# Kernel optimization log

Measured on AMD Instinct MI355X. Metric: run time of the kernel, lower is better.

## Reference

```python
import jax, jax.numpy as jnp
import numpy as np

B, T, D_MODEL, D_HEAD = 4, 4096, 512, 64  # batch, token_depth, token_len, d_head
D_K = 64
NEG = -1.0e9  # mask fill value used by the torch module


def setup_inputs() -> dict:
    key = jax.random.key(0)
    kx, kq, kk, kv = jax.random.split(key, 4)
    x = jax.random.normal(kx, (B, T, D_MODEL), dtype=jnp.float32)
    # nn.Linear(token_len, d_head, bias=False) -> weight shape [d_head, token_len]
    Wq = jax.random.normal(kq, (D_HEAD, D_MODEL), dtype=jnp.float32) * 0.02
    Wk = jax.random.normal(kk, (D_HEAD, D_MODEL), dtype=jnp.float32) * 0.02
    Wv = jax.random.normal(kv, (D_HEAD, D_MODEL), dtype=jnp.float32) * 0.02
    return {"x": x, "Wq": Wq, "Wk": Wk, "Wv": Wv}


def reference(x, Wq, Wk, Wv):
    # q/k/v projections: y = x @ W.T  (Linear with bias=False)
    q = jnp.einsum("btd,hd->bth", x, Wq)  # [B,T,D_HEAD]
    k = jnp.einsum("btd,hd->bth", x, Wk)
    v = jnp.einsum("btd,hd->bth", x, Wv)

    scores = jnp.einsum("bth,bsh->bts", q, k)  # [B,T,T]

    # additive causal mask: upper triangle (diagonal=1) filled with -1e9
    t_idx = jnp.arange(T)
    mask = jnp.where(t_idx[None, :] > t_idx[:, None], NEG, 0.0).astype(scores.dtype)
    scores = scores + mask[None, :, :]

    sqrt_dk = jnp.sqrt(jnp.asarray(D_K, dtype=scores.dtype))
    # NOTE: original code applies softmax over dim=1 (the query axis), not -1.
    attn = jax.nn.softmax(scores / sqrt_dk, axis=1)
    out = jnp.einsum("bts,bsh->bth", attn, v)  # [B,T,D_HEAD]
    return out
```

## Files before the change

### kernel.cpp

```cpp
#include <hip/hip_runtime.h>

#define B_ 4
#define T_ 4096
#define DM 512
#define DH 64
#define CS 512
#define CTS 1024

typedef short short8 __attribute__((ext_vector_type(8)));
typedef short bf16x4 __attribute__((ext_vector_type(4)));
typedef float f32x4 __attribute__((ext_vector_type(4)));
typedef float float8 __attribute__((ext_vector_type(8)));

__device__ inline short f2bf(float f) {
    unsigned u = __float_as_uint(f);
    u += 0x7fffu + ((u >> 16) & 1u);
    return (short)(u >> 16);
}
__device__ inline float bf2f(short s) {
    return __uint_as_float(((unsigned)(unsigned short)s) << 16);
}
__device__ inline short8 cvt8(const float* p) {
    float8 v = *(const float8*)p;
    short8 r;
#pragma unroll
    for (int j = 0; j < 8; j++) r[j] = f2bf(v[j]);
    return r;
}
__device__ inline unsigned cvt_pk_bf16(float a, float b) {
    unsigned r;
    asm("v_cvt_pk_bf16_f32 %0, %1, %2" : "=v"(r) : "v"(a), "v"(b));
    return r;
}
__device__ inline bf16x4 pmask4(f32x4 d, int sbase, int t) {
    float p[4];
#pragma unroll
    for (int r = 0; r < 4; r++) {
        float e = __expf(d[r] * 0.125f);
        p[r] = (sbase + r <= t) ? e : 0.f;
    }
    union { unsigned u[2]; bf16x4 v; } z;
    z.u[0] = cvt_pk_bf16(p[0], p[1]);
    z.u[1] = cvt_pk_bf16(p[2], p[3]);
    return z.v;
}

__global__ __launch_bounds__(256) void k_wcvt(
    const float* __restrict__ Wq, const float* __restrict__ Wk,
    const float* __restrict__ Wv, short* __restrict__ wb)
{
    int e = (blockIdx.x * 256 + threadIdx.x) * 8;
    int m = e / (DH * DM);
    int off = e - m * (DH * DM);
    const float* W = (m == 0) ? Wq : (m == 1) ? Wk : Wv;
    *(short8*)(wb + e) = cvt8(W + off);
}

__global__ __launch_bounds__(256, 4) void k_proj(
    const float* __restrict__ x, const short* __restrict__ wb,
    short* __restrict__ qb, short* __restrict__ kb, short* __restrict__ vb)
{
    __shared__ short Xs[64 * 72];
    __shared__ short Ws[192 * 72];
    int tid = threadIdx.x;
    int lane = tid & 63, w = tid >> 6;
    int l16 = lane & 15, quad = lane >> 4;
    int b = blockIdx.x >> 6;
    int tile = blockIdx.x & 63;
    int t0 = tile * 64;
    long xbase = ((long)(b * T_ + t0)) * DM;

    f32x4 acc[12];
#pragma unroll
    for (int i = 0; i < 12; i++) acc[i] = (f32x4)(0.f);

    for (int kc = 0; kc < DM; kc += 64) {
#pragma unroll
        for (int p = 0; p < 2; p++) {
            int idx = p * 256 + tid;
            int row = idx >> 3, col = (idx & 7) * 8;
            *(short8*)(Xs + row * 72 + col) = cvt8(x + xbase + (long)row * DM + kc + col);
        }
#pragma unroll
        for (int p = 0; p < 6; p++) {
            int idx = p * 256 + tid;
            int row = idx >> 3, col = (idx & 7) * 8;
            *(short8*)(Ws + row * 72 + col) =
                *(const short8*)(wb + (long)row * DM + kc + col);
        }
        __syncthreads();
#pragma unroll
        for (int ks = 0; ks < 2; ks++) {
            short8 af = *(const short8*)(Xs + (w * 16 + l16) * 72 + ks * 32 + quad * 8);
#pragma unroll
            for (int hh = 0; hh < 12; hh++) {
                short8 bf = *(const short8*)(Ws + (hh * 16 + l16) * 72 + ks * 32 + quad * 8);
                acc[hh] = __builtin_amdgcn_mfma_f32_16x16x32_bf16(af, bf, acc[hh], 0, 0, 0);
            }
        }
        __syncthreads();
    }
#pragma unroll
    for (int m = 0; m < 3; m++) {
        short* outp = (m == 0) ? qb : (m == 1) ? kb : vb;
#pragma unroll
        for (int h4 = 0; h4 < 4; h4++)
#pragma unroll
            for (int r4 = 0; r4 < 4; r4++) {
                int t = t0 + w * 16 + quad * 4 + r4;
                outp[((long)(b * T_ + t)) * DH + h4 * 16 + l16] = f2bf(acc[m * 4 + h4][r4]);
            }
    }
}

__global__ __launch_bounds__(256, 4) void k_stats(
    const short* __restrict__ qb, const short* __restrict__ kb, float* __restrict__ lsum)
{
    __shared__ short Qb[128 * 72];
    int tid = threadIdx.x;
    int lane = tid & 63, w = tid >> 6;
    int l16 = lane & 15, quad = lane >> 4;
    const int NC = T_ / CTS;
    int chunk = blockIdx.x % NC;
    int st = (blockIdx.x / NC) & 31;
    int b = blockIdx.x / (NC * 32);
    int c0 = chunk * CTS, cend = c0 + CTS;
    int s0blk = st * 128;
    if (cend <= s0blk) return;
    int s0w = s0blk + w * 32;
    long bq = (long)b * T_ * DH;

    const short8* kp0 = (const short8*)(kb + bq + (long)(s0w + l16) * DH + quad * 8);
    short8 a00 = kp0[0], a01 = kp0[4];
    const short8* kp1 = (const short8*)(kb + bq + (long)(s0w + 16 + l16) * DH + quad * 8);
    short8 a10 = kp1[0], a11 = kp1[4];

    int t_lo = (c0 > s0blk) ? c0 : s0blk;
    int nsteps = (cend - t_lo) >> 7;
    float acc0[4] = {0.f, 0.f, 0.f, 0.f};
    float acc1[4] = {0.f, 0.f, 0.f, 0.f};

    for (int stp = 0; stp < nsteps; stp++) {
        int t0 = t_lo + stp * 128;
#pragma unroll
        for (int p = 0; p < 4; p++) {
            int idx = p * 256 + tid;
            int row = idx >> 3, col = idx & 7;
            *(short8*)(Qb + row * 72 + col * 8) =
                *(const short8*)(qb + bq + (long)(t0 + row) * DH + col * 8);
        }
        __syncthreads();
        for (int sub = 0; sub < 8; sub++) {
            int tt = t0 + sub * 16;
            if (tt + 15 >= s0w) {
                short8 b0 = *(const short8*)(Qb + (sub * 16 + l16) * 72 + quad * 8);
                short8 b1 = *(const short8*)(Qb + (sub * 16 + l16) * 72 + 32 + quad * 8);
                int t = tt + l16;
                f32x4 d0 = (f32x4)(0.f);
                d0 = __builtin_amdgcn_mfma_f32_16x16x32_bf16(a00, b0, d0, 0, 0, 0);
                d0 = __builtin_amdgcn_mfma_f32_16x16x32_bf16(a01, b1, d0, 0, 0, 0);
#pragma unroll
                for (int r = 0; r < 4; r++) {
                    int s = s0w + quad * 4 + r;
                    float p = __expf(d0[r] * 0.125f);
                    acc0[r] += (t >= s) ? p : 0.f;
                }
                if (tt + 15 >= s0w + 16) {
                    f32x4 d1 = (f32x4)(0.f);
                    d1 = __builtin_amdgcn_mfma_f32_16x16x32_bf16(a10, b0, d1, 0, 0, 0);
                    d1 = __builtin_amdgcn_mfma_f32_16x16x32_bf16(a11, b1, d1, 0, 0, 0);
#pragma unroll
                    for (int r = 0; r < 4; r++) {
                        int s = s0w + 16 + quad * 4 + r;
                        float p = __expf(d1[r] * 0.125f);
                        acc1[r] += (t >= s) ? p : 0.f;
                    }
                }
            }
        }
        __syncthreads();
    }
#pragma unroll
    for (int r = 0; r < 4; r++) {
        float v = acc0[r];
        v += __shfl_xor(v, 1, 16); v += __shfl_xor(v, 2, 16);
        v += __shfl_xor(v, 4, 16); v += __shfl_xor(v, 8, 16);
        if (l16 == 0) atomicAdd(&lsum[b * T_ + s0w + quad * 4 + r], v);
        float v1 = acc1[r];
        v1 += __shfl_xor(v1, 1, 16); v1 += __shfl_xor(v1, 2, 16);
        v1 += __shfl_xor(v1, 4, 16); v1 += __shfl_xor(v1, 8, 16);
        if (l16 == 0) atomicAdd(&lsum[b * T_ + s0w + 16 + quad * 4 + r], v1);
    }
}

__global__ __launch_bounds__(256) void k_vt(
    const short* __restrict__ vb, const float* __restrict__ lsum, short* __restrict__ vTc)
{
    int tid = threadIdx.x;
    int b = blockIdx.x >> 6;
    int s0 = (blockIdx.x & 63) * 64;
    int h = tid & 63, g = tid >> 6;
    long vbase = ((long)(b * T_) + s0 + g * 16) * DH + h;
    long lbase = (long)b * T_ + s0 + g * 16;
    short8 lo, hi;
#pragma unroll
    for (int k2 = 0; k2 < 8; k2++) {
        float rl = 1.0f / lsum[lbase + k2];
        lo[k2] = f2bf(bf2f(vb[vbase + (long)k2 * DH]) * rl);
        float rh = 1.0f / lsum[lbase + 8 + k2];
        hi[k2] = f2bf(bf2f(vb[vbase + (long)(8 + k2) * DH]) * rh);
    }
    long ob = ((long)(b * 256 + (s0 >> 4) + g) * 64 + h) * 16;
    *(short8*)(vTc + ob) = lo;
    *(short8*)(vTc + ob + 8) = hi;
}

__global__ __launch_bounds__(256, 4) void k_out(
    const short* __restrict__ qb, const short* __restrict__ kb,
    const short* __restrict__ vTc, float* __restrict__ out)
{
    __shared__ short Kb[128 * 72];
    __shared__ short Vb[8 * 64 * 20];
    int tid = threadIdx.x;
    int lane = tid & 63, w = tid >> 6;
    int l16 = lane & 15, quad = lane >> 4;
    const int NC = T_ / CS;
    int chunk = blockIdx.x % NC;
    int strip = (blockIdx.x / NC) & 31;
    int b = blockIdx.x / (NC * 32);
    int c0 = chunk * CS;
    int blk_tmax = strip * 128 + 127;
    if (c0 > blk_tmax) return;
    int s_hi = (c0 + CS < blk_tmax + 1) ? c0 + CS : blk_tmax + 1;
    int nsteps = (s_hi - c0 + 127) >> 7;
    int t0w = strip * 128 + w * 32;
    long bq = (long)b * T_ * DH;

    const short8* qp0 = (const short8*)(qb + bq + (long)(t0w + l16) * DH + quad * 8);
    short8 q00 = qp0[0], q01 = qp0[4];
    const short8* qp1 = (const short8*)(qb + bq + (long)(t0w + 16 + l16) * DH + quad * 8);
    short8 q10 = qp1[0], q11 = qp1[4];
    const short* vTb = vTc + (long)b * (T_ / 16) * DH * 16;

    f32x4 o0[4], o1[4];
#pragma unroll
    for (int i = 0; i < 4; i++) { o0[i] = (f32x4)(0.f); o1[i] = (f32x4)(0.f); }
    int t0 = t0w + l16, t1 = t0 + 16;

    for (int stp = 0; stp < nsteps; stp++) {
        int s0 = c0 + stp * 128;
#pragma unroll
        for (int p = 0; p < 4; p++) {
            int idx = p * 256 + tid;
            int row = idx >> 3, col = idx & 7;
            *(short8*)(Kb + row * 72 + col * 8) =
                *(const short8*)(kb + bq + (long)(s0 + row) * DH + col * 8);
        }
        int g0 = s0 >> 4;
#pragma unroll
        for (int p = 0; p < 4; p++) {
            int idx = p * 256 + tid;
            int g = idx >> 7, rem = idx & 127;
            int h = rem >> 1, c = rem & 1;
            const short* src = vTb + (long)(g0 + g) * 1024 + h * 16 + c * 8;
            short* dst = Vb + g * 1280 + h * 20 + c * 8;
            *(bf16x4*)(dst) = *(const bf16x4*)(src);
            *(bf16x4*)(dst + 4) = *(const bf16x4*)(src + 4);
        }
        __syncthreads();

        for (int sub = 0; sub < 8; sub++) {
            int sc = s0 + sub * 16;
            if (sc > t0w + 31) break;
            short8 a0 = *(const short8*)(Kb + (sub * 16 + l16) * 72 + quad * 8);
            short8 a1 = *(const short8*)(Kb + (sub * 16 + l16) * 72 + 32 + quad * 8);

            f32x4 d1 = (f32x4)(0.f);
            d1 = __builtin_amdgcn_mfma_f32_16x16x32_bf16(a0, q10, d1, 0, 0, 0);
            d1 = __builtin_amdgcn_mfma_f32_16x16x32_bf16(a1, q11, d1, 0, 0, 0);
            bf16x4 pa1 = pmask4(d1, sc + quad * 4, t1);

            bf16x4 pa0 = (bf16x4)(short)0;
            if (sc <= t0w + 15) {
                f32x4 d0 = (f32x4)(0.f);
                d0 = __builtin_amdgcn_mfma_f32_16x16x32_bf16(a0, q00, d0, 0, 0, 0);
                d0 = __builtin_amdgcn_mfma_f32_16x16x32_bf16(a1, q01, d0, 0, 0, 0);
                pa0 = pmask4(d0, sc + quad * 4, t0);
            }
            const short* vc = Vb + sub * 1280 + quad * 4;
#pragma unroll
            for (int h4 = 0; h4 < 4; h4++) {
                bf16x4 bv = *(const bf16x4*)(vc + (h4 * 16 + l16) * 20);
                o1[h4] = __builtin_amdgcn_mfma_f32_16x16x16bf16_1k(pa1, bv, o1[h4], 0, 0, 0);
                o0[h4] = __builtin_amdgcn_mfma_f32_16x16x16bf16_1k(pa0, bv, o0[h4], 0, 0, 0);
            }
        }
        __syncthreads();
    }
#pragma unroll
    for (int h4 = 0; h4 < 4; h4++)
#pragma unroll
        for (int r = 0; r < 4; r++) {
            int t = t0w + quad * 4 + r;
            atomicAdd(&out[bq + (long)t * DH + h4 * 16 + l16], o0[h4][r]);
            atomicAdd(&out[bq + (long)(t + 16) * DH + h4 * 16 + l16], o1[h4][r]);
        }
}

extern "C" void kernel_launch(void* const* d_in, const int* in_sizes, int n_in,
                              void* d_out, int out_size, void* d_ws, size_t ws_size,
                              hipStream_t stream) {
    const float* x  = (const float*)d_in[0];
    const float* Wq = (const float*)d_in[1];
    const float* Wk = (const float*)d_in[2];
    const float* Wv = (const float*)d_in[3];
    float* out = (float*)d_out;

    char* ws = (char*)d_ws;
    short* qb   = (short*)(ws);
    short* kb   = (short*)(ws + (2l << 20));
    short* vb   = (short*)(ws + (4l << 20));
    short* vTc  = (short*)(ws + (6l << 20));
    short* wb   = (short*)(ws + (8l << 20));
    float* lsum = (float*)(ws + (9l << 20));

    hipMemsetAsync(out, 0, (size_t)out_size * sizeof(float), stream);
    hipMemsetAsync(lsum, 0, (size_t)(B_ * T_) * sizeof(float), stream);

    k_wcvt<<<dim3(48), dim3(256), 0, stream>>>(Wq, Wk, Wv, wb);
    k_proj<<<dim3(B_ * T_ / 64), dim3(256), 0, stream>>>(x, wb, qb, kb, vb);
    k_stats<<<dim3(B_ * 32 * (T_ / CTS)), dim3(256), 0, stream>>>(qb, kb, lsum);
    k_vt<<<dim3(B_ * T_ / 64), dim3(256), 0, stream>>>(vb, lsum, vTc);
    k_out<<<dim3(B_ * 32 * (T_ / CS)), dim3(256), 0, stream>>>(qb, kb, vTc, out);
}
```

Baseline: 166.7 us.

## Shrink projection tiles, halve stats chunk size, read V directly from global

The projection kernel now uses 16-token tiles with each wave computing 3 of the 12 head tiles, which gives four times as many blocks to fill more CUs. The stats kernel's key chunk size drops from 1024 to 512, adding parallelism and atomic partial sums. The output kernel no longer stages V into shared memory and instead loads bf16x4 fragments straight from global/L2 inside the inner loop. The goal is higher occupancy and less LDS traffic, at the cost of reloading weights more often in the projection and taking uncached global-load latency in the attention inner loop.

```diff
diff --git a/kernel.cpp b/kernel.cpp
--- a/kernel.cpp
+++ b/kernel.cpp
@@ -5,7 +5,7 @@
 #define DM 512
 #define DH 64
 #define CS 512
-#define CTS 1024
+#define CTS 512
 
 typedef short short8 __attribute__((ext_vector_type(8)));
 typedef short bf16x4 __attribute__((ext_vector_type(4)));
@@ -60,25 +60,24 @@
     const float* __restrict__ x, const short* __restrict__ wb,
     short* __restrict__ qb, short* __restrict__ kb, short* __restrict__ vb)
 {
-    __shared__ short Xs[64 * 72];
+    __shared__ short Xs[16 * 72];
     __shared__ short Ws[192 * 72];
     int tid = threadIdx.x;
     int lane = tid & 63, w = tid >> 6;
     int l16 = lane & 15, quad = lane >> 4;
-    int b = blockIdx.x >> 6;
-    int tile = blockIdx.x & 63;
-    int t0 = tile * 64;
+    int b = blockIdx.x >> 8;
+    int tile = blockIdx.x & 255;
+    int t0 = tile * 16;
     long xbase = ((long)(b * T_ + t0)) * DM;
-
-    f32x4 acc[12];
-#pragma unroll
-    for (int i = 0; i < 12; i++) acc[i] = (f32x4)(0.f);
+    int hb = w * 3;
+
+    f32x4 acc[3];
+#pragma unroll
+    for (int i = 0; i < 3; i++) acc[i] = (f32x4)(0.f);
 
     for (int kc = 0; kc < DM; kc += 64) {
-#pragma unroll
-        for (int p = 0; p < 2; p++) {
-            int idx = p * 256 + tid;
-            int row = idx >> 3, col = (idx & 7) * 8;
+        if (tid < 128) {
+            int row = tid >> 3, col = (tid & 7) * 8;
             *(short8*)(Xs + row * 72 + col) = cvt8(x + xbase + (long)row * DM + kc + col);
         }
 #pragma unroll
@@ -91,25 +90,24 @@
         __syncthreads();
 #pragma unroll
         for (int ks = 0; ks < 2; ks++) {
-            short8 af = *(const short8*)(Xs + (w * 16 + l16) * 72 + ks * 32 + quad * 8);
-#pragma unroll
-            for (int hh = 0; hh < 12; hh++) {
-                short8 bf = *(const short8*)(Ws + (hh * 16 + l16) * 72 + ks * 32 + quad * 8);
-                acc[hh] = __builtin_amdgcn_mfma_f32_16x16x32_bf16(af, bf, acc[hh], 0, 0, 0);
+            short8 af = *(const short8*)(Xs + l16 * 72 + ks * 32 + quad * 8);
+#pragma unroll
+            for (int j = 0; j < 3; j++) {
+                short8 bf = *(const short8*)(Ws + ((hb + j) * 16 + l16) * 72 + ks * 32 + quad * 8);
+                acc[j] = __builtin_amdgcn_mfma_f32_16x16x32_bf16(af, bf, acc[j], 0, 0, 0);
             }
         }
         __syncthreads();
     }
 #pragma unroll
-    for (int m = 0; m < 3; m++) {
+    for (int j = 0; j < 3; j++) {
+        int hh = hb + j, m = hh >> 2, h4 = hh & 3;
         short* outp = (m == 0) ? qb : (m == 1) ? kb : vb;
 #pragma unroll
-        for (int h4 = 0; h4 < 4; h4++)
-#pragma unroll
-            for (int r4 = 0; r4 < 4; r4++) {
-                int t = t0 + w * 16 + quad * 4 + r4;
-                outp[((long)(b * T_ + t)) * DH + h4 * 16 + l16] = f2bf(acc[m * 4 + h4][r4]);
-            }
+        for (int r4 = 0; r4 < 4; r4++) {
+            int t = t0 + quad * 4 + r4;
+            outp[((long)(b * T_ + t)) * DH + h4 * 16 + l16] = f2bf(acc[j][r4]);
+        }
     }
 }
 
@@ -220,7 +218,6 @@
     const short* __restrict__ vTc, float* __restrict__ out)
 {
     __shared__ short Kb[128 * 72];
-    __shared__ short Vb[8 * 64 * 20];
     int tid = threadIdx.x;
     int lane = tid & 63, w = tid >> 6;
     int l16 = lane & 15, quad = lane >> 4;
@@ -256,17 +253,6 @@
             *(short8*)(Kb + row * 72 + col * 8) =
                 *(const short8*)(kb + bq + (long)(s0 + row) * DH + col * 8);
         }
-        int g0 = s0 >> 4;
-#pragma unroll
-        for (int p = 0; p < 4; p++) {
-            int idx = p * 256 + tid;
-            int g = idx >> 7, rem = idx & 127;
-            int h = rem >> 1, c = rem & 1;
-            const short* src = vTb + (long)(g0 + g) * 1024 + h * 16 + c * 8;
-            short* dst = Vb + g * 1280 + h * 20 + c * 8;
-            *(bf16x4*)(dst) = *(const bf16x4*)(src);
-            *(bf16x4*)(dst + 4) = *(const bf16x4*)(src + 4);
-        }
         __syncthreads();
 
         for (int sub = 0; sub < 8; sub++) {
@@ -287,10 +273,10 @@
                 d0 = __builtin_amdgcn_mfma_f32_16x16x32_bf16(a1, q01, d0, 0, 0, 0);
                 pa0 = pmask4(d0, sc + quad * 4, t0);
             }
-            const short* vc = Vb + sub * 1280 + quad * 4;
+            const short* vc = vTb + (long)((sc) >> 4) * 1024 + quad * 4;
 #pragma unroll
             for (int h4 = 0; h4 < 4; h4++) {
-                bf16x4 bv = *(const bf16x4*)(vc + (h4 * 16 + l16) * 20);
+                bf16x4 bv = *(const bf16x4*)(vc + (h4 * 16 + l16) * 16);
                 o1[h4] = __builtin_amdgcn_mfma_f32_16x16x16bf16_1k(pa1, bv, o1[h4], 0, 0, 0);
                 o0[h4] = __builtin_amdgcn_mfma_f32_16x16x16bf16_1k(pa0, bv, o0[h4], 0, 0, 0);
             }
@@ -328,7 +314,7 @@
     hipMemsetAsync(lsum, 0, (size_t)(B_ * T_) * sizeof(float), stream);
 
     k_wcvt<<<dim3(48), dim3(256), 0, stream>>>(Wq, Wk, Wv, wb);
-    k_proj<<<dim3(B_ * T_ / 64), dim3(256), 0, stream>>>(x, wb, qb, kb, vb);
+    k_proj<<<dim3(B_ * T_ / 16), dim3(256), 0, stream>>>(x, wb, qb, kb, vb);
     k_stats<<<dim3(B_ * 32 * (T_ / CTS)), dim3(256), 0, stream>>>(qb, kb, lsum);
     k_vt<<<dim3(B_ * T_ / 64), dim3(256), 0, stream>>>(vb, lsum, vTc);
     k_out<<<dim3(B_ * 32 * (T_ / CS)), dim3(256), 0, stream>>>(qb, kb, vTc, out);
```

After: 150.3 us. -9.8%, faster.
